# Kernel optimization log

Measured on AMD Instinct MI355X. Metric: run time of the kernel, lower is better.

Reference implementation:

```python
import jax, jax.numpy as jnp
import numpy as np
import math

HEAD_DIM = 256
NUM_HEADS = 8
NUM_KV_HEADS = 1
ROPE_THETA = 10000.0


def _rope_cos_sin(position_ids, dim, base, dtype):
    # inv_freq: [dim//2]
    inv_freq = 1.0 / (base ** (jnp.arange(0, dim, 2, dtype=jnp.float32) / dim))
    # freqs: [B, S, dim//2]
    freqs = position_ids.astype(jnp.float32)[..., None] * inv_freq[None, None, :]
    emb = jnp.concatenate([freqs, freqs], axis=-1)  # [B, S, dim]
    return jnp.cos(emb).astype(dtype), jnp.sin(emb).astype(dtype)


def _rotate_half(x):
    half = x.shape[-1] // 2
    return jnp.concatenate([-x[..., half:], x[..., :half]], axis=-1)


def setup_inputs() -> dict:
    key = jax.random.key(0)
    ks = jax.random.split(key, 6)
    B, S, H = 2, 2048, 2048
    hidden_states = jax.random.normal(ks[0], (B, S, H), dtype=jnp.float32)
    attention_mask = jnp.zeros((B, 1, S, S), dtype=jnp.float32)
    position_ids = jnp.arange(B * S, dtype=jnp.int64).reshape(B, S) % S
    wq = jax.random.normal(ks[1], (H, NUM_HEADS * HEAD_DIM), dtype=jnp.float32) * 0.02
    wk = jax.random.normal(ks[2], (H, NUM_KV_HEADS * HEAD_DIM), dtype=jnp.float32) * 0.02
    wv = jax.random.normal(ks[3], (H, NUM_KV_HEADS * HEAD_DIM), dtype=jnp.float32) * 0.02
    wo = jax.random.normal(ks[4], (NUM_HEADS * HEAD_DIM, H), dtype=jnp.float32) * 0.02
    return {"hidden_states": hidden_states, "attention_mask": attention_mask,
            "position_ids": position_ids, "wq": wq, "wk": wk, "wv": wv, "wo": wo}


def reference(hidden_states, attention_mask, position_ids, wq, wk, wv, wo):
    B, S, _ = hidden_states.shape
    q = (hidden_states @ wq).reshape(B, S, NUM_HEADS, HEAD_DIM).transpose(0, 2, 1, 3)
    k = (hidden_states @ wk).reshape(B, S, NUM_KV_HEADS, HEAD_DIM).transpose(0, 2, 1, 3)
    v = (hidden_states @ wv).reshape(B, S, NUM_KV_HEADS, HEAD_DIM).transpose(0, 2, 1, 3)

    cos, sin = _rope_cos_sin(position_ids, HEAD_DIM, ROPE_THETA, hidden_states.dtype)
    cos = cos[:, None, :, :]  # [B,1,S,D]
    sin = sin[:, None, :, :]
    q = q * cos + _rotate_half(q) * sin
    k = k * cos + _rotate_half(k) * sin

    # repeat_kv (GQA/MQA expansion)
    n_rep = NUM_HEADS // NUM_KV_HEADS
    k = jnp.repeat(k, n_rep, axis=1)  # [B,H,S,D]
    v = jnp.repeat(v, n_rep, axis=1)

    scores = jnp.einsum('bhqd,bhkd->bhqk', q, k) / math.sqrt(HEAD_DIM)
    scores = scores + attention_mask
    probs = jax.nn.softmax(scores.astype(jnp.float32), axis=-1).astype(q.dtype)
    attn = jnp.einsum('bhqk,bhkd->bhqd', probs, v)  # [B,H,S,D]
    attn = attn.transpose(0, 2, 1, 3).reshape(B, S, NUM_HEADS * HEAD_DIM)
    return attn @ wo
```

## Files before the change

kernel.cpp:

```cpp
#include <hip/hip_runtime.h>
#include <hip/hip_bf16.h>

typedef unsigned short u16;
using f32x4  = __attribute__((ext_vector_type(4))) float;
using bf16x8 = __attribute__((ext_vector_type(8))) __bf16;
using u16x8  = __attribute__((ext_vector_type(8))) unsigned short;
using u16x4  = __attribute__((ext_vector_type(4))) unsigned short;

__device__ __forceinline__ float bf2f(u16 v) {
  union { unsigned u; float f; } x; x.u = ((unsigned)v) << 16; return x.f;
}
__device__ __forceinline__ u16 f2bf(float f) {
  union { float f; unsigned u; } x; x.f = f;
  unsigned r = x.u + 0x7fffu + ((x.u >> 16) & 1u);
  return (u16)(r >> 16);
}
__device__ __forceinline__ void async_load16(const u16* g, u16* l) {
  __builtin_amdgcn_global_load_lds(
      (const __attribute__((address_space(1))) unsigned int*)g,
      (__attribute__((address_space(3))) unsigned int*)l, 16, 0, 0);
}
__device__ __forceinline__ float fexp2(float x) {
#if __has_builtin(__builtin_amdgcn_exp2f)
  return __builtin_amdgcn_exp2f(x);
#else
  return exp2f(x);
#endif
}
__device__ __forceinline__ float vmax4(f32x4 v) {
  return fmaxf(fmaxf(v[0], v[1]), fmaxf(v[2], v[3]));
}
__device__ __forceinline__ int swz_col(int col, int rowk) {
  return (col & ~63) | ((((col >> 3) & 7) ^ rowk) << 3) | (col & 7);
}

__global__ __launch_bounds__(256) void cast_f32_bf16_sw(const float* __restrict__ in,
                                                        u16* __restrict__ out) {
  long i = ((long)blockIdx.x * 256 + threadIdx.x) * 8;
  int m = (int)(i >> 11);
  int col = (int)(i & 2047);
  float4 a = *(const float4*)(in + i);
  float4 b = *(const float4*)(in + i + 4);
  u16x8 v;
  v[0] = f2bf(a.x); v[1] = f2bf(a.y); v[2] = f2bf(a.z); v[3] = f2bf(a.w);
  v[4] = f2bf(b.x); v[5] = f2bf(b.y); v[6] = f2bf(b.z); v[7] = f2bf(b.w);
  *(u16x8*)(out + ((long)m << 11) + swz_col(col, m & 7)) = v;
}

__global__ __launch_bounds__(256) void trans_all(const float* __restrict__ wq,
                                                 const float* __restrict__ wk,
                                                 const float* __restrict__ wv,
                                                 const float* __restrict__ wo,
                                                 u16* __restrict__ wqkvT, u16* __restrict__ woT) {
  const int z = blockIdx.z, bx = blockIdx.x, by = blockIdx.y;
  if (z == 1 && bx >= 64) return;
  const float* src; int srs; u16* dst;
  const int R0 = bx * 32;
  if (z == 0) {
    if (R0 < 2048)      { src = wq + R0;          srs = 2048; }
    else if (R0 < 2304) { src = wk + (R0 - 2048); srs = 256;  }
    else                { src = wv + (R0 - 2304); srs = 256;  }
    dst = wqkvT;
  } else { src = wo + R0; srs = 2048; dst = woT; }
  __shared__ float t[32][33];
  int tx = threadIdx.x, ty = threadIdx.y;
  int br = by * 32;
#pragma unroll
  for (int i = 0; i < 32; i += 8)
    t[ty + i][tx] = src[(long)(br + ty + i) * srs + tx];
  __syncthreads();
#pragma unroll
  for (int i = 0; i < 32; i += 8) {
    int R = R0 + ty + i, C = br + tx;
    dst[(long)R * 2048 + swz_col(C, R & 7)] = f2bf(t[tx][ty + i]);
  }
}

template <int NTW, typename CT>
__global__ __launch_bounds__(512, 2) void gemm_v4(const u16* __restrict__ A,
                                                  const u16* __restrict__ Bt,
                                                  CT* __restrict__ C, int M, int N, int K) {
  constexpr int BN  = NTW * 64;
  constexpr int RT  = 128 + BN;
  constexpr int CPW = RT / 64;
  __shared__ __attribute__((aligned(16))) u16 sBuf[2][RT * 64];
  const int n0 = blockIdx.x * BN, m0 = blockIdx.y * 128;
  const int tid = threadIdx.x;
  const int w = tid >> 6, lane = tid & 63;
  const int l15 = lane & 15, quad = lane >> 4;
  const int wm = (w >> 2) * 64, wn = (w & 3) * (NTW * 16);
  const int lrow = lane >> 3, lcol = (lane & 7) * 8;
  const u16* Ag = A + (long)(m0 + lrow) * K + lcol;
  const u16* Bg = Bt + (long)(n0 + lrow) * K + lcol;
  const int g0 = ((quad ^ (l15 & 7)) << 3);
  f32x4 acc[4][NTW] = {};

  const auto stage = [&](int t, int bf) {
    const int k0 = t * 64;
#pragma unroll
    for (int j = 0; j < CPW; ++j) {
      const int chunk = w * CPW + j;
      const u16* src = (chunk < 16)
          ? (Ag + (long)(chunk * 8) * K + k0)
          : (Bg + (long)((chunk - 16) * 8) * K + k0);
      async_load16(src, &sBuf[bf][chunk * 512]);
    }
  };

  stage(0, 0);
  __syncthreads();

  const int T = K >> 6;
  for (int t = 0; t < T; ++t) {
    const int cur = t & 1;
    if (t + 1 < T) stage(t + 1, cur ^ 1);
#pragma unroll
    for (int kk = 0; kk < 2; ++kk) {
      const int g = kk ? (g0 ^ 32) : g0;
      bf16x8 af[4], bfr[NTW];
#pragma unroll
      for (int mt = 0; mt < 4; ++mt)
        af[mt] = *(const bf16x8*)&sBuf[cur][(wm + mt * 16 + l15) * 64 + g];
#pragma unroll
      for (int nt = 0; nt < NTW; ++nt)
        bfr[nt] = *(const bf16x8*)&sBuf[cur][(128 + wn + nt * 16 + l15) * 64 + g];
      __builtin_amdgcn_s_setprio(1);
#pragma unroll
      for (int mt = 0; mt < 4; ++mt)
#pragma unroll
        for (int nt = 0; nt < NTW; ++nt)
          acc[mt][nt] = __builtin_amdgcn_mfma_f32_16x16x32_bf16(af[mt], bfr[nt], acc[mt][nt], 0, 0, 0);
      __builtin_amdgcn_s_setprio(0);
    }
    __syncthreads();
  }
#pragma unroll
  for (int mt = 0; mt < 4; ++mt)
#pragma unroll
    for (int nt = 0; nt < NTW; ++nt)
#pragma unroll
      for (int r = 0; r < 4; ++r) {
        long idx = (long)(m0 + wm + mt * 16 + quad * 4 + r) * N + (n0 + wn + nt * 16 + l15);
        if constexpr (sizeof(CT) == 4) C[idx] = acc[mt][nt][r];
        else                           C[idx] = f2bf(acc[mt][nt][r]);
      }
}

__global__ __launch_bounds__(256) void rope_pack(u16* __restrict__ qkv, u16* __restrict__ kp) {
  const int row = blockIdx.x;
  const int tid = threadIdx.x;
  const int d = tid & 127;
  const int s = row & 2047;
  float ang = (float)s * fexp2(-(float)d * 0.10381025296523007f);
  float sn, cs;
  sincosf(ang, &sn, &cs);
  long base = (long)row * 2560;
#pragma unroll
  for (int j = 0; j < 4; ++j) {
    int h = (tid >> 7) + j * 2;
    long p = base + h * 256 + d;
    float x0 = bf2f(qkv[p]), x1 = bf2f(qkv[p + 128]);
    qkv[p]       = f2bf(x0 * cs - x1 * sn);
    qkv[p + 128] = f2bf(x1 * cs + x0 * sn);
  }
  if (tid < 128) {
    long p = base + 2048 + d;
    float x0 = bf2f(qkv[p]), x1 = bf2f(qkv[p + 128]);
    float y0 = x0 * cs - x1 * sn, y1 = x1 * cs + x0 * sn;
    int b = row >> 11, t = (row >> 6) & 31, r = row & 63;
    long sw = (r >> 1) & 7;
    long tb = (long)(b * 32 + t) * 8 * 2048;
#pragma unroll
    for (int u = 0; u < 2; ++u) {
      int D = d + u * 128;
      long off = tb + (long)(D >> 5) * 2048 + r * 32 + (D & 31);
      long off2 = (((off >> 3) ^ sw) << 3) | (off & 7);
      kp[off2] = f2bf(u ? y1 : y0);
    }
  }
}

__global__ __launch_bounds__(256) void pack_vt(const u16* __restrict__ qkv, u16* __restrict__ vp) {
  __shared__ u16 sm[32][40];
  int x = blockIdx.x, y = blockIdx.y, b = blockIdx.z;
  int tx = threadIdx.x, ty = threadIdx.y;
  long inrow = (long)b * 2048 + (y >> 1) * 64 + (y & 1) * 32;
#pragma unroll
  for (int i = 0; i < 32; i += 8)
    sm[ty + i][tx] = qkv[(inrow + ty + i) * 2560 + 2304 + x * 32 + tx];
  __syncthreads();
  long obase = ((long)(b * 32 + (y >> 1)) * 2 + (y & 1)) * 8192 + (long)x * 1024;
#pragma unroll
  for (int i = 0; i < 32; i += 8) {
    long el = obase + (ty + i) * 32 + tx;
    el ^= (long)((((ty + i) >> 1) & 7) << 3);
    vp[el] = sm[tx][ty + i];
  }
}

__global__ __launch_bounds__(512) void flash_attn(const u16* __restrict__ qkv,
                                                  const u16* __restrict__ kp,
                                                  const u16* __restrict__ vp,
                                                  u16* __restrict__ attn) {
  const int qt = blockIdx.x, h = blockIdx.y, b = blockIdx.z;
  const int tid = threadIdx.x, w = tid >> 6, lane = tid & 63;
  const int l15 = lane & 15, quad = lane >> 4;
  __shared__ __attribute__((aligned(16))) u16 sK[2][16384];
  __shared__ __attribute__((aligned(16))) u16 sV[2][16384];
  __shared__ __attribute__((aligned(16))) u16 sP[8][1152];
  const long rowb = (long)b * 2048;
  const int qrow0 = qt * 128 + w * 16;
  const int swz_rd = (l15 >> 1) * 64 + ((((l15 & 1) << 2) | quad) ^ (l15 >> 1)) * 8;

  bf16x8 aq[8];
  {
    const u16* qp = qkv + (rowb + qrow0 + l15) * 2560 + h * 256 + quad * 8;
#pragma unroll
    for (int kk = 0; kk < 8; ++kk) aq[kk] = *(const bf16x8*)(qp + kk * 32);
  }

  float m_i = -1e30f, l_i = 0.f;
  f32x4 accO[16] = {};
  const float SC = 0.09016844005556021f;

  u16* Pw = &sP[w][0];
  const u16* kpb = kp + (long)b * 32 * 16384;
  const u16* vpb = vp + (long)b * 32 * 16384;

#pragma unroll
  for (int j = 0; j < 4; ++j) {
    int base = (w * 4 + j) * 512;
    async_load16(kpb + base + lane * 8, &sK[0][base]);
    async_load16(vpb + base + lane * 8, &sV[0][base]);
  }
  __syncthreads();

  for (int it = 0; it < 32; ++it) {
    const int cur = it & 1;
    const int nx = (it < 31) ? it + 1 : 31;
    const u16* ktn = kpb + (long)nx * 16384;
    const u16* vtn = vpb + (long)nx * 16384;
#pragma unroll
    for (int j = 0; j < 4; ++j) {
      int base = (w * 4 + j) * 512;
      async_load16(ktn + base + lane * 8, &sK[cur ^ 1][base]);
      async_load16(vtn + base + lane * 8, &sV[cur ^ 1][base]);
    }
    f32x4 sc[4] = {};
#pragma unroll
    for (int kk = 0; kk < 8; ++kk)
#pragma unroll
      for (int nt = 0; nt < 2; ++nt) {
        bf16x8 bk = *(const bf16x8*)&sK[cur][kk * 2048 + nt * 512 + swz_rd];
        sc[nt] = __builtin_amdgcn_mfma_f32_16x16x32_bf16(bk, aq[kk], sc[nt], 0, 0, 0);
      }
#pragma unroll
    for (int kk = 0; kk < 8; ++kk)
#pragma unroll
      for (int nt = 2; nt < 4; ++nt) {
        bf16x8 bk = *(const bf16x8*)&sK[cur][kk * 2048 + nt * 512 + swz_rd];
        sc[nt] = __builtin_amdgcn_mfma_f32_16x16x32_bf16(bk, aq[kk], sc[nt], 0, 0, 0);
      }

    {
      float mx = fmaxf(vmax4(sc[0]), vmax4(sc[1])) * SC;
      float s1 = __shfl_xor(mx, 16, 64);
      float s2 = __shfl_xor(mx, 32, 64);
      float s3 = __shfl_xor(mx, 48, 64);
      mx = fmaxf(fmaxf(mx, s1), fmaxf(s2, s3));
      if (!__all(mx - m_i <= 8.f)) {
        float mnew = fmaxf(m_i, mx);
        float al = fexp2(m_i - mnew);
        m_i = mnew;
        l_i *= al;
#pragma unroll
        for (int r = 0; r < 4; ++r) {
          float ar = __shfl(al, quad * 4 + r, 16);
#pragma unroll
          for (int t = 0; t < 16; ++t) accO[t][r] *= ar;
        }
      }
      float rs = 0.f;
#pragma unroll
      for (int nt = 0; nt < 2; ++nt) {
        u16x4 pk;
#pragma unroll
        for (int r = 0; r < 4; ++r) {
          float pv = fexp2(sc[nt][r] * SC - m_i);
          rs += pv;
          pk[r] = f2bf(pv);
        }
        *(u16x4*)&Pw[l15 * 72 + nt * 16 + quad * 4] = pk;
      }
      l_i += rs;
    }
    asm volatile("s_waitcnt lgkmcnt(0)" ::: "memory");
    bf16x8 pa0 = *(const bf16x8*)&Pw[l15 * 72 + quad * 8];
#pragma unroll
    for (int t = 0; t < 16; ++t) {
      bf16x8 bv0 = *(const bf16x8*)&sV[cur][t * 512 + swz_rd];
      accO[t] = __builtin_amdgcn_mfma_f32_16x16x32_bf16(pa0, bv0, accO[t], 0, 0, 0);
    }
    {
      float mx = fmaxf(vmax4(sc[2]), vmax4(sc[3])) * SC;
      float s1 = __shfl_xor(mx, 16, 64);
      float s2 = __shfl_xor(mx, 32, 64);
      float s3 = __shfl_xor(mx, 48, 64);
      mx = fmaxf(fmaxf(mx, s1), fmaxf(s2, s3));
      if (!__all(mx - m_i <= 8.f)) {
        float mnew = fmaxf(m_i, mx);
        float al = fexp2(m_i - mnew);
        m_i = mnew;
        l_i *= al;
#pragma unroll
        for (int r = 0; r < 4; ++r) {
          float ar = __shfl(al, quad * 4 + r, 16);
#pragma unroll
          for (int t = 0; t < 16; ++t) accO[t][r] *= ar;
        }
      }
      float rs = 0.f;
#pragma unroll
      for (int nt = 2; nt < 4; ++nt) {
        u16x4 pk;
#pragma unroll
        for (int r = 0; r < 4; ++r) {
          float pv = fexp2(sc[nt][r] * SC - m_i);
          rs += pv;
          pk[r] = f2bf(pv);
        }
        *(u16x4*)&Pw[l15 * 72 + nt * 16 + quad * 4] = pk;
      }
      l_i += rs;
    }
    asm volatile("s_waitcnt lgkmcnt(0)" ::: "memory");
    bf16x8 pa1 = *(const bf16x8*)&Pw[l15 * 72 + 32 + quad * 8];
#pragma unroll
    for (int t = 0; t < 16; ++t) {
      bf16x8 bv1 = *(const bf16x8*)&sV[cur][8192 + t * 512 + swz_rd];
      accO[t] = __builtin_amdgcn_mfma_f32_16x16x32_bf16(pa1, bv1, accO[t], 0, 0, 0);
    }
    __syncthreads();
  }
  {
    float t1 = __shfl_xor(l_i, 16, 64);
    float t2 = __shfl_xor(l_i, 32, 64);
    float t3 = __shfl_xor(l_i, 48, 64);
    l_i = (l_i + t1) + (t2 + t3);
  }
#pragma unroll
  for (int r = 0; r < 4; ++r) {
    float lr = __shfl(l_i, quad * 4 + r, 16);
    float rinv = 1.f / lr;
    int key = (quad * 4 + r) & 7;
#pragma unroll
    for (int t = 0; t < 16; ++t) {
      int col = h * 256 + t * 16 + l15;
      attn[(rowb + qrow0 + quad * 4 + r) * 2048 + swz_col(col, key)] =
          f2bf(accO[t][r] * rinv);
    }
  }
}

extern "C" void kernel_launch(void* const* d_in, const int* in_sizes, int n_in,
                              void* d_out, int out_size, void* d_ws, size_t ws_size,
                              hipStream_t stream) {
  const float* hidden = (const float*)d_in[0];
  const float* wq = (const float*)d_in[3];
  const float* wk = (const float*)d_in[4];
  const float* wv = (const float*)d_in[5];
  const float* wo = (const float*)d_in[6];
  float* out = (float*)d_out;

  char* ws = (char*)d_ws;
  u16* QKV   = (u16*)(ws);
  u16* WqkvT = (u16*)(ws + 20971520);
  u16* Kp    = (u16*)(ws + 20971520);
  u16* Vp    = (u16*)(ws + 23068672);
  u16* WoT   = (u16*)(ws + 31457280);
  u16* HB    = (u16*)(ws + 39845888);
  u16* ATT   = (u16*)(ws + 39845888);

  cast_f32_bf16_sw<<<4096, 256, 0, stream>>>(hidden, HB);
  trans_all<<<dim3(80, 64, 2), dim3(32, 8), 0, stream>>>(wq, wk, wv, wo, WqkvT, WoT);

  gemm_v4<5, u16><<<dim3(8, 32), dim3(512), 0, stream>>>(HB, WqkvT, QKV, 4096, 2560, 2048);

  rope_pack<<<4096, 256, 0, stream>>>(QKV, Kp);
  pack_vt<<<dim3(8, 64, 2), dim3(32, 8), 0, stream>>>(QKV, Vp);

  flash_attn<<<dim3(16, 8, 2), dim3(512), 0, stream>>>(QKV, Kp, Vp, ATT);

  gemm_v4<4, float><<<dim3(8, 32), dim3(512), 0, stream>>>(ATT, WoT, out, 4096, 2048, 2048);
}
```

Before: 338.8 us.

## Use 256x256 GEMM tiles with XCD-aware block-to-tile mapping

Replaces the 128xBN GEMM tile with a 256x256 tile per 512-thread block, where each wave computes a 64x128 sub-tile. This raises arithmetic intensity per LDS byte loaded. A 1D grid is remapped so that blocks on the same XCD share M rows, for better L2 reuse. The cost is fewer blocks (160 and 128 on 256 CUs, so some CUs sit idle), more accumulator registers (128 floats per lane), and 64KB of LDS per buffer pair, which likely limits occupancy to one block per CU.

Result: slower. 348.9 us (+3.0%).

```diff
diff --git a/kernel.cpp b/kernel.cpp
--- a/kernel.cpp
+++ b/kernel.cpp
@@ -76,33 +76,35 @@
   }
 }
 
-template <int NTW, typename CT>
-__global__ __launch_bounds__(512, 2) void gemm_v4(const u16* __restrict__ A,
+template <typename CT>
+__global__ __launch_bounds__(512, 2) void gemm_v5(const u16* __restrict__ A,
                                                   const u16* __restrict__ Bt,
-                                                  CT* __restrict__ C, int M, int N, int K) {
-  constexpr int BN  = NTW * 64;
-  constexpr int RT  = 128 + BN;
-  constexpr int CPW = RT / 64;
-  __shared__ __attribute__((aligned(16))) u16 sBuf[2][RT * 64];
-  const int n0 = blockIdx.x * BN, m0 = blockIdx.y * 128;
+                                                  CT* __restrict__ C, int M, int N, int K,
+                                                  int nNb) {
+  __shared__ __attribute__((aligned(16))) u16 sBuf[2][512 * 64];
+  const int bid = blockIdx.x;
+  const int xcd = bid & 7, kk_ = bid >> 3;
+  const int mb = xcd * 2 + kk_ / nNb;
+  const int nb = kk_ - (kk_ / nNb) * nNb;
+  const int m0 = mb * 256, n0 = nb * 256;
   const int tid = threadIdx.x;
   const int w = tid >> 6, lane = tid & 63;
   const int l15 = lane & 15, quad = lane >> 4;
-  const int wm = (w >> 2) * 64, wn = (w & 3) * (NTW * 16);
+  const int wm = (w >> 1) * 64, wn = (w & 1) * 128;
   const int lrow = lane >> 3, lcol = (lane & 7) * 8;
   const u16* Ag = A + (long)(m0 + lrow) * K + lcol;
   const u16* Bg = Bt + (long)(n0 + lrow) * K + lcol;
   const int g0 = ((quad ^ (l15 & 7)) << 3);
-  f32x4 acc[4][NTW] = {};
+  f32x4 acc[4][8] = {};
 
   const auto stage = [&](int t, int bf) {
     const int k0 = t * 64;
 #pragma unroll
-    for (int j = 0; j < CPW; ++j) {
-      const int chunk = w * CPW + j;
-      const u16* src = (chunk < 16)
+    for (int j = 0; j < 8; ++j) {
+      const int chunk = w * 8 + j;
+      const u16* src = (chunk < 32)
           ? (Ag + (long)(chunk * 8) * K + k0)
-          : (Bg + (long)((chunk - 16) * 8) * K + k0);
+          : (Bg + (long)((chunk - 32) * 8) * K + k0);
       async_load16(src, &sBuf[bf][chunk * 512]);
     }
   };
@@ -117,18 +119,18 @@
 #pragma unroll
     for (int kk = 0; kk < 2; ++kk) {
       const int g = kk ? (g0 ^ 32) : g0;
-      bf16x8 af[4], bfr[NTW];
+      bf16x8 af[4], bfr[8];
 #pragma unroll
       for (int mt = 0; mt < 4; ++mt)
         af[mt] = *(const bf16x8*)&sBuf[cur][(wm + mt * 16 + l15) * 64 + g];
 #pragma unroll
-      for (int nt = 0; nt < NTW; ++nt)
-        bfr[nt] = *(const bf16x8*)&sBuf[cur][(128 + wn + nt * 16 + l15) * 64 + g];
+      for (int nt = 0; nt < 8; ++nt)
+        bfr[nt] = *(const bf16x8*)&sBuf[cur][(256 + wn + nt * 16 + l15) * 64 + g];
       __builtin_amdgcn_s_setprio(1);
 #pragma unroll
       for (int mt = 0; mt < 4; ++mt)
 #pragma unroll
-        for (int nt = 0; nt < NTW; ++nt)
+        for (int nt = 0; nt < 8; ++nt)
           acc[mt][nt] = __builtin_amdgcn_mfma_f32_16x16x32_bf16(af[mt], bfr[nt], acc[mt][nt], 0, 0, 0);
       __builtin_amdgcn_s_setprio(0);
     }
@@ -137,7 +139,7 @@
 #pragma unroll
   for (int mt = 0; mt < 4; ++mt)
 #pragma unroll
-    for (int nt = 0; nt < NTW; ++nt)
+    for (int nt = 0; nt < 8; ++nt)
 #pragma unroll
       for (int r = 0; r < 4; ++r) {
         long idx = (long)(m0 + wm + mt * 16 + quad * 4 + r) * N + (n0 + wn + nt * 16 + l15);
@@ -384,12 +386,12 @@
   cast_f32_bf16_sw<<<4096, 256, 0, stream>>>(hidden, HB);
   trans_all<<<dim3(80, 64, 2), dim3(32, 8), 0, stream>>>(wq, wk, wv, wo, WqkvT, WoT);
 
-  gemm_v4<5, u16><<<dim3(8, 32), dim3(512), 0, stream>>>(HB, WqkvT, QKV, 4096, 2560, 2048);
+  gemm_v5<u16><<<160, 512, 0, stream>>>(HB, WqkvT, QKV, 4096, 2560, 2048, 10);
 
   rope_pack<<<4096, 256, 0, stream>>>(QKV, Kp);
   pack_vt<<<dim3(8, 64, 2), dim3(32, 8), 0, stream>>>(QKV, Vp);
 
   flash_attn<<<dim3(16, 8, 2), dim3(512), 0, stream>>>(QKV, Kp, Vp, ATT);
 
-  gemm_v4<4, float><<<dim3(8, 32), dim3(512), 0, stream>>>(ATT, WoT, out, 4096, 2048, 2048);
-}
+  gemm_v5<float><<<128, 512, 0, stream>>>(ATT, WoT, out, 4096, 2048, 2048, 8);
+}
```
